# Kernel optimization log

Hardware: AMD Instinct MI355X
Metric: run time of the kernel (lower is better)

The kernel has to match this reference:

```python
import jax, jax.numpy as jnp
import numpy as np

N = 100000
E = 3200000
IN_C = 256
HID = 64
OUT_C = 2
EPS = 1e-5


def setup_inputs() -> dict:
    key = jax.random.key(0)
    ks = jax.random.split(key, 8)
    x = jax.random.normal(ks[0], (N, IN_C), dtype=jnp.float32)
    edge_index = jax.random.randint(ks[1], (2, E), 0, N, dtype=jnp.int64)
    # GCNConv weights (PyG: out = A_hat @ (x W) + b)
    W1 = jax.random.normal(ks[2], (IN_C, HID), dtype=jnp.float32) / np.sqrt(IN_C)
    b1 = jnp.zeros((HID,), dtype=jnp.float32)
    W2 = jax.random.normal(ks[3], (HID, OUT_C), dtype=jnp.float32) / np.sqrt(HID)
    b2 = jnp.zeros((OUT_C,), dtype=jnp.float32)
    # BatchNorm affine params
    g1 = jnp.ones((HID,), dtype=jnp.float32)
    be1 = jnp.zeros((HID,), dtype=jnp.float32)
    g2 = jnp.ones((OUT_C,), dtype=jnp.float32)
    be2 = jnp.zeros((OUT_C,), dtype=jnp.float32)
    # Decoder linear
    Wd = jax.random.normal(ks[4], (OUT_C, IN_C), dtype=jnp.float32) / np.sqrt(OUT_C)
    bd = jnp.zeros((IN_C,), dtype=jnp.float32)
    return {"x": x, "edge_index": edge_index, "W1": W1, "b1": b1, "g1": g1,
            "be1": be1, "W2": W2, "b2": b2, "g2": g2, "be2": be2,
            "Wd": Wd, "bd": bd}


def gcn_conv(x, W, b, src, dst, n):
    # x: [N, Cin] -> [N, Cout]; symmetric-normalized aggregation with self-loops
    xw = x @ W  # [N, Cout]
    loops = jnp.arange(n, dtype=src.dtype)
    s = jnp.concatenate([src, loops])  # [E+N]
    d = jnp.concatenate([dst, loops])
    deg = jax.ops.segment_sum(jnp.ones_like(d, dtype=x.dtype), d, num_segments=n)
    dinv = jax.lax.rsqrt(deg)  # deg >= 1 thanks to self-loops
    norm = dinv[s] * dinv[d]   # [E+N]
    out = jax.ops.segment_sum(norm[:, None] * xw[s], d, num_segments=n)
    return out + b


def batch_norm(x, gamma, beta):
    # training-mode BN over node dim, biased variance (torch semantics)
    mu = jnp.mean(x, axis=0)
    var = jnp.mean(jnp.square(x - mu), axis=0)
    return (x - mu) * jax.lax.rsqrt(var + EPS) * gamma + beta


def reference(x, edge_index, W1, b1, g1, be1, W2, b2, g2, be2, Wd, bd):
    src, dst = edge_index[0], edge_index[1]
    n = x.shape[0]
    h = gcn_conv(x, W1, b1, src, dst, n)
    h = jax.nn.relu(batch_norm(h, g1, be1))
    # dropout: identity (inference)
    z = batch_norm(gcn_conv(h, W2, b2, src, dst, n), g2, be2)
    return z @ Wd + bd  # decoder: [N, IN_C]
```

## Files before the change

### kernel.cpp

```cpp
#include <hip/hip_runtime.h>
#include <hip/hip_bf16.h>

#define NN 100000
#define NE 3200000
#define INC 256
#define HID 64
#define OUTC 2
#define EPSV 1e-5f

#define SCAN_CHUNK 1024
#define NBLK ((NN + SCAN_CHUNK - 1) / SCAN_CHUNK)

#define NBUCK 128
#define BCAP  26000
#define BIN_CHUNK 4096
#define BIN_K 16
#define BIN_GRID ((NE + BIN_CHUNK - 1) / BIN_CHUNK)

#define NHALF 50000

typedef short short8 __attribute__((ext_vector_type(8)));
typedef float f32x4 __attribute__((ext_vector_type(4)));

static __device__ __forceinline__ float bf2f(unsigned short u) {
    return __uint_as_float((unsigned)u << 16);
}
static __device__ __forceinline__ unsigned short f2bf(float f) {
    __hip_bfloat16 hb = __float2bfloat16(f);
    return *(unsigned short*)&hb;
}

__global__ __launch_bounds__(256) void bin_kernel(const int* __restrict__ src,
                                                  const int* __restrict__ dst,
                                                  int* __restrict__ gtail,
                                                  int2* __restrict__ bbuf) {
    __shared__ int bcnt[NBUCK], bbase[NBUCK];
    int t = threadIdx.x;
    if (t < NBUCK) bcnt[t] = 0;
    __syncthreads();
    int base = blockIdx.x * BIN_CHUNK;
    int s[BIN_K], d[BIN_K], sl[BIN_K], bk[BIN_K];
#pragma unroll
    for (int r = 0; r < BIN_K; r++) {
        int i = base + r * 256 + t;
        bool v = i < NE;
        s[r] = v ? src[i] : 0;
        d[r] = v ? dst[i] : 0;
        bk[r] = (int)(((unsigned)d[r] * (unsigned)NBUCK) / (unsigned)NN);
        sl[r] = v ? atomicAdd(&bcnt[bk[r]], 1) : 0;
    }
    __syncthreads();
    if (t < NBUCK) bbase[t] = bcnt[t] ? atomicAdd(&gtail[t], bcnt[t]) : 0;
    __syncthreads();
#pragma unroll
    for (int r = 0; r < BIN_K; r++) {
        int i = base + r * 256 + t;
        if (i < NE) {
            int b = bk[r];
            bbuf[(size_t)b * BCAP + bbase[b] + sl[r]] = make_int2(s[r], d[r]);
        }
    }
}

__global__ __launch_bounds__(256) void hist2_kernel(const int2* __restrict__ bbuf,
                                                    const int* __restrict__ gtail,
                                                    int* __restrict__ cnt) {
    __shared__ int h[800];
    int b = blockIdx.x, t = threadIdx.x;
    int nb = (b * NN + NBUCK - 1) >> 7;
    int ne_ = ((b + 1) * NN + NBUCK - 1) >> 7;
    int range = ne_ - nb;
    for (int i = t; i < range; i += 256) h[i] = 0;
    __syncthreads();
    int ecnt = gtail[b];
    const int2* p = bbuf + (size_t)b * BCAP;
    for (int i = t; i < ecnt; i += 256) {
        int2 e = p[i];
        atomicAdd(&h[e.y - nb], 1);
    }
    __syncthreads();
    for (int i = t; i < range; i += 256) cnt[nb + i] = h[i];
}

__global__ void scan_btot_kernel(const int* __restrict__ cnt, int* __restrict__ btot) {
    __shared__ int red[4];
    int b = blockIdx.x, t = threadIdx.x;
    int base = b * SCAN_CHUNK;
    int v = 0;
    for (int j = t; j < SCAN_CHUNK; j += 256) {
        int idx = base + j;
        v += (idx < NN) ? cnt[idx] : 0;
    }
    for (int o = 32; o; o >>= 1) v += __shfl_xor(v, o);
    int wave = t >> 6, lane = t & 63;
    if (lane == 0) red[wave] = v;
    __syncthreads();
    if (t == 0) btot[b] = red[0] + red[1] + red[2] + red[3];
}

__global__ void scan_boff_kernel(const int* __restrict__ btot, int* __restrict__ boff) {
    __shared__ int wtot[2];
    int t = threadIdx.x;
    int lane = t & 63, wave = t >> 6;
    int v = (t < NBLK) ? btot[t] : 0;
    int s = v;
    for (int o = 1; o < 64; o <<= 1) {
        int u = __shfl_up(s, o);
        if (lane >= o) s += u;
    }
    if (lane == 63) wtot[wave] = s;
    __syncthreads();
    int add = (wave == 1) ? wtot[0] : 0;
    if (t < NBLK) boff[t] = s - v + add;
}

__global__ void scan_rowptr_kernel(const int* __restrict__ cnt, const int* __restrict__ boff,
                                   int* __restrict__ rowptr, float* __restrict__ dinv) {
    __shared__ int wsum[4];
    int b = blockIdx.x, t = threadIdx.x;
    int lane = t & 63, wave = t >> 6;
    int idx = b * SCAN_CHUNK + t * 4;
    int c0 = (idx + 0 < NN) ? cnt[idx + 0] : 0;
    int c1 = (idx + 1 < NN) ? cnt[idx + 1] : 0;
    int c2 = (idx + 2 < NN) ? cnt[idx + 2] : 0;
    int c3 = (idx + 3 < NN) ? cnt[idx + 3] : 0;
    int local = c0 + c1 + c2 + c3;
    int s = local;
    for (int o = 1; o < 64; o <<= 1) {
        int u = __shfl_up(s, o);
        if (lane >= o) s += u;
    }
    if (lane == 63) wsum[wave] = s;
    __syncthreads();
    if (t == 0) {
        int run = 0;
        for (int w = 0; w < 4; w++) { int x = wsum[w]; wsum[w] = run; run += x; }
    }
    __syncthreads();
    int start = boff[b] + wsum[wave] + (s - local);
    if (idx + 0 < NN) { rowptr[idx + 0] = start;                dinv[idx + 0] = rsqrtf((float)(c0 + 1)); }
    if (idx + 1 < NN) { rowptr[idx + 1] = start + c0;           dinv[idx + 1] = rsqrtf((float)(c1 + 1)); }
    if (idx + 2 < NN) { rowptr[idx + 2] = start + c0 + c1;      dinv[idx + 2] = rsqrtf((float)(c2 + 1)); }
    if (idx + 3 < NN) { rowptr[idx + 3] = start + c0 + c1 + c2; dinv[idx + 3] = rsqrtf((float)(c3 + 1)); }
    if (b == 0 && t == 0) rowptr[NN] = NE;
}

__global__ __launch_bounds__(256) void scatter2_kernel(const int2* __restrict__ bbuf,
                                                       const int* __restrict__ gtail,
                                                       const int* __restrict__ rowptr,
                                                       int* __restrict__ e_src) {
    __shared__ int fill[800];
    int b = blockIdx.x, t = threadIdx.x;
    int nb = (b * NN + NBUCK - 1) >> 7;
    int ne_ = ((b + 1) * NN + NBUCK - 1) >> 7;
    int range = ne_ - nb;
    for (int i = t; i < range; i += 256) fill[i] = 0;
    __syncthreads();
    int ecnt = gtail[b];
    const int2* p = bbuf + (size_t)b * BCAP;
    for (int i = t; i < ecnt; i += 256) {
        int2 e = p[i];
        int pos = rowptr[e.y] + atomicAdd(&fill[e.y - nb], 1);
        e_src[pos] = e.x;
    }
}

__global__ __launch_bounds__(256) void wprep_kernel(const float* __restrict__ W1,
                                                    unsigned short* __restrict__ Wtb) {
    int t = blockIdx.x * 256 + threadIdx.x;
    int c = t & 63;
    int k = t >> 6;
    Wtb[c * 256 + k] = f2bf(W1[k * 64 + c]);
}

#define G1_ROWS 32
#define LDP 264
__global__ __launch_bounds__(256) void gemm1_kernel(const float* __restrict__ x,
                                                    const unsigned short* __restrict__ Wtb,
                                                    const float* __restrict__ dinv,
                                                    unsigned short* __restrict__ xw1p) {
    __shared__ unsigned short xt[G1_ROWS * LDP];
    __shared__ unsigned short wt[HID * LDP];
    int t = threadIdx.x;
    size_t base = (size_t)blockIdx.x * G1_ROWS;

    const float4* xg = (const float4*)(x + base * INC);
#pragma unroll
    for (int ii = 0; ii < 8; ii++) {
        int idx4 = ii * 256 + t;
        float4 v = xg[idx4];
        int f = idx4 * 4;
        int row = f >> 8, k = f & 255;
        ushort4 u;
        u.x = f2bf(v.x); u.y = f2bf(v.y); u.z = f2bf(v.z); u.w = f2bf(v.w);
        *(ushort4*)(xt + row * LDP + k) = u;
    }
    const int4* wsrc = (const int4*)Wtb;
#pragma unroll
    for (int ii = 0; ii < 8; ii++) {
        int idx4 = ii * 256 + t;
        int4 v = wsrc[idx4];
        int e16 = idx4 * 8;
        int c = e16 >> 8, k = e16 & 255;
        *(int4*)(wt + c * LDP + k) = v;
    }
    __syncthreads();

    int lane = t & 63;
    int wave = t >> 6;
    int l15 = lane & 15;
    int hi = lane >> 4;
    int rgrp = wave & 1;
    int cgrp = wave >> 1;
    const unsigned short* ap = xt + (rgrp * 16 + l15) * LDP;
    const unsigned short* bp0 = wt + (cgrp * 32 + l15) * LDP;
    const unsigned short* bp1 = bp0 + 16 * LDP;
    f32x4 acc0 = {0.f, 0.f, 0.f, 0.f};
    f32x4 acc1 = {0.f, 0.f, 0.f, 0.f};
#pragma unroll
    for (int kk = 0; kk < 8; kk++) {
        int ko = kk * 32 + hi * 8;
        short8 a  = *(const short8*)(ap + ko);
        short8 b0 = *(const short8*)(bp0 + ko);
        short8 b1 = *(const short8*)(bp1 + ko);
        acc0 = __builtin_amdgcn_mfma_f32_16x16x32_bf16(a, b0, acc0, 0, 0, 0);
        acc1 = __builtin_amdgcn_mfma_f32_16x16x32_bf16(a, b1, acc1, 0, 0, 0);
    }
    unsigned short* p0 = xw1p + (size_t)(cgrp * 2) * NN * 16;
    unsigned short* p1 = p0 + (size_t)NN * 16;
#pragma unroll
    for (int i = 0; i < 4; i++) {
        int grow = (int)base + rgrp * 16 + hi * 4 + i;
        float dv = dinv[grow];
        p0[(size_t)grow * 16 + l15] = f2bf(acc0[i] * dv);
        p1[(size_t)grow * 16 + l15] = f2bf(acc1[i] * dv);
    }
}

__global__ __launch_bounds__(256) void agg1_kernel(const unsigned short* __restrict__ xw1p,
                                                   const int* __restrict__ rowptr,
                                                   const int* __restrict__ e_src,
                                                   const float* __restrict__ dinv,
                                                   const float* __restrict__ b1,
                                                   float* __restrict__ h1p,
                                                   float* __restrict__ sums1) {
    __shared__ float lsum[4][16], lsq[4][16];
    int t = threadIdx.x;
    int lane = t & 63;
    int wave = t >> 6;
    int grp = lane >> 3;
    int cl = lane & 7;
    int cohort = blockIdx.x & 7;
    int q = cohort & 3;
    int h = cohort >> 2;
    const ushort2* plane = (const ushort2*)(xw1p + (size_t)q * NN * 16);
    float* hp = h1p + (size_t)q * NN * 16;
    float bb0 = b1[q * 16 + cl * 2 + 0];
    float bb1 = b1[q * 16 + cl * 2 + 1];
    int gid = ((blockIdx.x >> 3) * 4 + wave) * 8 + grp;
    int dlo = h * NHALF;
    float ssum0 = 0.f, ssq0 = 0.f, ssum1 = 0.f, ssq1 = 0.f;
    for (int d = dlo + gid; d < dlo + NHALF; d += 8192) {
        int beg = rowptr[d], end = rowptr[d + 1];
        float a0 = 0.f, a1 = 0.f;
        int e = beg;
        for (; e + 3 < end; e += 4) {
            int s0 = e_src[e], s1 = e_src[e + 1], s2 = e_src[e + 2], s3 = e_src[e + 3];
            ushort2 u0 = plane[(size_t)s0 * 8 + cl];
            ushort2 u1 = plane[(size_t)s1 * 8 + cl];
            ushort2 u2 = plane[(size_t)s2 * 8 + cl];
            ushort2 u3 = plane[(size_t)s3 * 8 + cl];
            a0 += bf2f(u0.x) + bf2f(u1.x) + bf2f(u2.x) + bf2f(u3.x);
            a1 += bf2f(u0.y) + bf2f(u1.y) + bf2f(u2.y) + bf2f(u3.y);
        }
        for (; e < end; e++) {
            int s = e_src[e];
            ushort2 u = plane[(size_t)s * 8 + cl];
            a0 += bf2f(u.x);
            a1 += bf2f(u.y);
        }
        ushort2 us = plane[(size_t)d * 8 + cl];
        a0 += bf2f(us.x);
        a1 += bf2f(us.y);
        float dv = dinv[d];
        float h0 = a0 * dv + bb0;
        float h1v = a1 * dv + bb1;
        *(float2*)(hp + (size_t)d * 16 + cl * 2) = make_float2(h0, h1v);
        ssum0 += h0; ssq0 += h0 * h0;
        ssum1 += h1v; ssq1 += h1v * h1v;
    }
    ssum0 += __shfl_xor(ssum0, 8);  ssum1 += __shfl_xor(ssum1, 8);
    ssq0  += __shfl_xor(ssq0, 8);   ssq1  += __shfl_xor(ssq1, 8);
    ssum0 += __shfl_xor(ssum0, 16); ssum1 += __shfl_xor(ssum1, 16);
    ssq0  += __shfl_xor(ssq0, 16);  ssq1  += __shfl_xor(ssq1, 16);
    ssum0 += __shfl_xor(ssum0, 32); ssum1 += __shfl_xor(ssum1, 32);
    ssq0  += __shfl_xor(ssq0, 32);  ssq1  += __shfl_xor(ssq1, 32);
    if (grp == 0) {
        lsum[wave][cl * 2] = ssum0; lsum[wave][cl * 2 + 1] = ssum1;
        lsq[wave][cl * 2]  = ssq0;  lsq[wave][cl * 2 + 1]  = ssq1;
    }
    __syncthreads();
    if (t < 16) {
        float S = lsum[0][t] + lsum[1][t] + lsum[2][t] + lsum[3][t];
        float Q = lsq[0][t] + lsq[1][t] + lsq[2][t] + lsq[3][t];
        atomicAdd(&sums1[q * 16 + t], S);
        atomicAdd(&sums1[64 + q * 16 + t], Q);
    }
}

__global__ __launch_bounds__(256) void gemm2_kernel(const float* __restrict__ h1p,
                                                    const float* __restrict__ sums1,
                                                    const float* __restrict__ g1,
                                                    const float* __restrict__ be1,
                                                    const float* __restrict__ W2,
                                                    const float* __restrict__ dinv,
                                                    float* __restrict__ xw2) {
    int lane = threadIdx.x & 63;
    int row = blockIdx.x * 4 + (threadIdx.x >> 6);
    if (row >= NN) return;
    int c = lane;
    const float invn = 1.0f / (float)NN;
    float mu = sums1[c] * invn;
    float var = sums1[64 + c] * invn - mu * mu;
    float sc = g1[c] * rsqrtf(var + EPSV);
    float sh = be1[c] - mu * sc;
    float hv = h1p[(size_t)(c >> 4) * NN * 16 + (size_t)row * 16 + (c & 15)] * sc + sh;
    hv = fmaxf(hv, 0.f);
    float p0 = hv * W2[c * 2 + 0];
    float p1 = hv * W2[c * 2 + 1];
    for (int o = 32; o; o >>= 1) {
        p0 += __shfl_xor(p0, o);
        p1 += __shfl_xor(p1, o);
    }
    if (lane == 0) {
        float dv = dinv[row];
        xw2[(size_t)row * 2 + 0] = p0 * dv;
        xw2[(size_t)row * 2 + 1] = p1 * dv;
    }
}

__global__ __launch_bounds__(256) void agg2_kernel(const float* __restrict__ xw2,
                                                   const int* __restrict__ rowptr,
                                                   const int* __restrict__ e_src,
                                                   const float* __restrict__ dinv,
                                                   const float* __restrict__ b2,
                                                   float* __restrict__ z2,
                                                   float* __restrict__ sums2) {
    __shared__ float red[4][4];
    int t = threadIdx.x;
    int lane = t & 63;
    int wave = t >> 6;
    int gl = lane & 7;
    int d = blockIdx.x * 32 + (t >> 3);
    int beg = rowptr[d], end = rowptr[d + 1];
    float a0 = 0.f, a1 = 0.f;
    int e = beg + gl;
    for (; e + 24 < end; e += 32) {
        int s0 = e_src[e], s1 = e_src[e + 8], s2 = e_src[e + 16], s3 = e_src[e + 24];
        float2 v0 = *(const float2*)(xw2 + (size_t)s0 * 2);
        float2 v1 = *(const float2*)(xw2 + (size_t)s1 * 2);
        float2 v2 = *(const float2*)(xw2 + (size_t)s2 * 2);
        float2 v3 = *(const float2*)(xw2 + (size_t)s3 * 2);
        a0 += v0.x + v1.x + v2.x + v3.x;
        a1 += v0.y + v1.y + v2.y + v3.y;
    }
    for (; e < end; e += 8) {
        int s = e_src[e];
        float2 v = *(const float2*)(xw2 + (size_t)s * 2);
        a0 += v.x;
        a1 += v.y;
    }
    if (gl == 0) {
        float2 sf = *(const float2*)(xw2 + (size_t)d * 2);
        a0 += sf.x;
        a1 += sf.y;
    }
    a0 += __shfl_xor(a0, 1); a1 += __shfl_xor(a1, 1);
    a0 += __shfl_xor(a0, 2); a1 += __shfl_xor(a1, 2);
    a0 += __shfl_xor(a0, 4); a1 += __shfl_xor(a1, 4);
    float dv = dinv[d];
    float z0 = a0 * dv + b2[0];
    float z1 = a1 * dv + b2[1];
    if (gl == 0) *(float2*)(z2 + (size_t)d * 2) = make_float2(z0, z1);
    float s0 = (gl == 0) ? z0 : 0.f;
    float s1 = (gl == 0) ? z1 : 0.f;
    float q0 = (gl == 0) ? z0 * z0 : 0.f;
    float q1 = (gl == 0) ? z1 * z1 : 0.f;
    for (int o = 8; o < 64; o <<= 1) {
        s0 += __shfl_xor(s0, o); s1 += __shfl_xor(s1, o);
        q0 += __shfl_xor(q0, o); q1 += __shfl_xor(q1, o);
    }
    if (lane == 0) { red[wave][0] = s0; red[wave][1] = s1; red[wave][2] = q0; red[wave][3] = q1; }
    __syncthreads();
    if (t < 4) {
        float v = red[0][t] + red[1][t] + red[2][t] + red[3][t];
        atomicAdd(&sums2[(blockIdx.x & 7) * 4 + t], v);
    }
}

__global__ __launch_bounds__(256) void decoder_kernel(const float* __restrict__ z2,
                                                      const float* __restrict__ sums2,
                                                      const float* __restrict__ g2,
                                                      const float* __restrict__ be2,
                                                      const float* __restrict__ Wd,
                                                      const float* __restrict__ bd,
                                                      float* __restrict__ out) {
    int g = blockIdx.x * 256 + threadIdx.x;
    int row = g >> 6;
    int c4 = (g & 63) * 4;
    float t0 = 0.f, t1 = 0.f, t2 = 0.f, t3 = 0.f;
#pragma unroll
    for (int bk = 0; bk < 8; bk++) {
        t0 += sums2[bk * 4 + 0]; t1 += sums2[bk * 4 + 1];
        t2 += sums2[bk * 4 + 2]; t3 += sums2[bk * 4 + 3];
    }
    const float invn = 1.0f / (float)NN;
    float mu0 = t0 * invn, mu1 = t1 * invn;
    float v0 = t2 * invn - mu0 * mu0;
    float v1 = t3 * invn - mu1 * mu1;
    float sc0 = g2[0] * rsqrtf(v0 + EPSV), sh0 = be2[0] - mu0 * sc0;
    float sc1 = g2[1] * rsqrtf(v1 + EPSV), sh1 = be2[1] - mu1 * sc1;
    float zb0 = z2[(size_t)row * 2 + 0] * sc0 + sh0;
    float zb1 = z2[(size_t)row * 2 + 1] * sc1 + sh1;
    float4 w0 = *(const float4*)(Wd + c4);
    float4 w1 = *(const float4*)(Wd + INC + c4);
    float4 bb = *(const float4*)(bd + c4);
    float4 o;
    o.x = zb0 * w0.x + zb1 * w1.x + bb.x;
    o.y = zb0 * w0.y + zb1 * w1.y + bb.y;
    o.z = zb0 * w0.z + zb1 * w1.z + bb.z;
    o.w = zb0 * w0.w + zb1 * w1.w + bb.w;
    *(float4*)(out + (size_t)row * INC + c4) = o;
}

static inline size_t align256(size_t x) { return (x + 255) & ~(size_t)255; }

extern "C" void kernel_launch(void* const* d_in, const int* in_sizes, int n_in,
                              void* d_out, int out_size, void* d_ws, size_t ws_size,
                              hipStream_t stream) {
    const float* x  = (const float*)d_in[0];
    const int*   ei = (const int*)d_in[1];
    const float* W1 = (const float*)d_in[2];
    const float* b1 = (const float*)d_in[3];
    const float* g1 = (const float*)d_in[4];
    const float* be1 = (const float*)d_in[5];
    const float* W2 = (const float*)d_in[6];
    const float* b2 = (const float*)d_in[7];
    const float* g2 = (const float*)d_in[8];
    const float* be2 = (const float*)d_in[9];
    const float* Wd = (const float*)d_in[10];
    const float* bd = (const float*)d_in[11];
    float* out = (float*)d_out;

    const int* src = ei;
    const int* dst = ei + NE;

    char* ws = (char*)d_ws;
    size_t off = 0;
    int* gtail = (int*)(ws + off);      off = align256(off + NBUCK * 4);
    float* sums1 = (float*)(ws + off);  off = align256(off + 128 * 4);
    float* sums2 = (float*)(ws + off);  off = align256(off + 32 * 4);
    size_t zero_bytes = off;
    int* cnt = (int*)(ws + off);        off = align256(off + NN * 4);
    int* rowptr = (int*)(ws + off);     off = align256(off + (NN + 1) * 4);
    float* dinv = (float*)(ws + off);   off = align256(off + NN * 4);
    int* btot = (int*)(ws + off);       off = align256(off + NBLK * 4);
    int* boff = (int*)(ws + off);       off = align256(off + NBLK * 4);
    unsigned short* Wtb = (unsigned short*)(ws + off); off = align256(off + (size_t)HID * INC * 2);
    int2* bbuf = (int2*)(ws + off);     off = align256(off + (size_t)NBUCK * BCAP * 8);
    int* e_src = (int*)(ws + off);      off = align256(off + (size_t)NE * 4 + 64);
    unsigned short* xw1p = (unsigned short*)(ws + off); off = align256(off + (size_t)NN * HID * 2);
    float* h1p = (float*)(ws + off);    off = align256(off + (size_t)NN * HID * 4);
    float* xw2 = (float*)(ws + off);    off = align256(off + (size_t)NN * 2 * 4);
    float* z2 = (float*)(ws + off);     off = align256(off + (size_t)NN * 2 * 4);
    (void)ws_size; (void)in_sizes; (void)n_in; (void)out_size;

    hipMemsetAsync(d_ws, 0, zero_bytes, stream);

    bin_kernel<<<BIN_GRID, 256, 0, stream>>>(src, dst, gtail, bbuf);
    hist2_kernel<<<NBUCK, 256, 0, stream>>>(bbuf, gtail, cnt);
    scan_btot_kernel<<<NBLK, 256, 0, stream>>>(cnt, btot);
    scan_boff_kernel<<<1, 128, 0, stream>>>(btot, boff);
    scan_rowptr_kernel<<<NBLK, 256, 0, stream>>>(cnt, boff, rowptr, dinv);
    scatter2_kernel<<<NBUCK, 256, 0, stream>>>(bbuf, gtail, rowptr, e_src);
    wprep_kernel<<<64, 256, 0, stream>>>(W1, Wtb);
    gemm1_kernel<<<NN / G1_ROWS, 256, 0, stream>>>(x, Wtb, dinv, xw1p);
    agg1_kernel<<<2048, 256, 0, stream>>>(xw1p, rowptr, e_src, dinv, b1, h1p, sums1);
    gemm2_kernel<<<(NN + 3) / 4, 256, 0, stream>>>(h1p, sums1, g1, be1, W2, dinv, xw2);
    agg2_kernel<<<NN * 8 / 256, 256, 0, stream>>>(xw2, rowptr, e_src, dinv, b2, z2, sums2);
    decoder_kernel<<<(NN * HID) / 256, 256, 0, stream>>>(z2, sums2, g2, be2, Wd, bd, out);
}
```

Baseline: 322.0 us.

## Split layer-1 features into two 32-channel planes for wider gathers

The bf16 XW1 intermediate and the fp32 h1 buffer change from four 16-channel planes to two 32-channel planes. Each aggregation thread now gathers 8 bytes (four channels) per neighbour instead of 4 bytes, and each cohort of blocks covers a quarter of the destination nodes instead of a half. The aim is fewer edge-index reads and row-pointer walks per feature and wider, more efficient gather transactions. In exchange each cohort's source plane is twice as large, so it may get less cache reuse, and each thread holds more registers.

Measured after the change: 317.4 us. Within noise of the previous version (-1.4%).

```diff
diff --git a/kernel.cpp b/kernel.cpp
--- a/kernel.cpp
+++ b/kernel.cpp
@@ -17,7 +17,7 @@
 #define BIN_K 16
 #define BIN_GRID ((NE + BIN_CHUNK - 1) / BIN_CHUNK)
 
-#define NHALF 50000
+#define NQUART 25000
 
 typedef short short8 __attribute__((ext_vector_type(8)));
 typedef float f32x4 __attribute__((ext_vector_type(4)));
@@ -178,7 +178,7 @@
 __global__ __launch_bounds__(256) void gemm1_kernel(const float* __restrict__ x,
                                                     const unsigned short* __restrict__ Wtb,
                                                     const float* __restrict__ dinv,
-                                                    unsigned short* __restrict__ xw1p) {
+                                                    unsigned short* __restrict__ xw1h) {
     __shared__ unsigned short xt[G1_ROWS * LDP];
     __shared__ unsigned short wt[HID * LDP];
     int t = threadIdx.x;
@@ -226,89 +226,99 @@
         acc0 = __builtin_amdgcn_mfma_f32_16x16x32_bf16(a, b0, acc0, 0, 0, 0);
         acc1 = __builtin_amdgcn_mfma_f32_16x16x32_bf16(a, b1, acc1, 0, 0, 0);
     }
-    unsigned short* p0 = xw1p + (size_t)(cgrp * 2) * NN * 16;
-    unsigned short* p1 = p0 + (size_t)NN * 16;
+    unsigned short* ph = xw1h + (size_t)cgrp * NN * 32;
 #pragma unroll
     for (int i = 0; i < 4; i++) {
         int grow = (int)base + rgrp * 16 + hi * 4 + i;
         float dv = dinv[grow];
-        p0[(size_t)grow * 16 + l15] = f2bf(acc0[i] * dv);
-        p1[(size_t)grow * 16 + l15] = f2bf(acc1[i] * dv);
-    }
-}
-
-__global__ __launch_bounds__(256) void agg1_kernel(const unsigned short* __restrict__ xw1p,
+        ph[(size_t)grow * 32 + l15]      = f2bf(acc0[i] * dv);
+        ph[(size_t)grow * 32 + l15 + 16] = f2bf(acc1[i] * dv);
+    }
+}
+
+__global__ __launch_bounds__(256) void agg1_kernel(const unsigned short* __restrict__ xw1h,
                                                    const int* __restrict__ rowptr,
                                                    const int* __restrict__ e_src,
                                                    const float* __restrict__ dinv,
                                                    const float* __restrict__ b1,
-                                                   float* __restrict__ h1p,
+                                                   float* __restrict__ h1h,
                                                    float* __restrict__ sums1) {
-    __shared__ float lsum[4][16], lsq[4][16];
+    __shared__ float lsum[4][32], lsq[4][32];
     int t = threadIdx.x;
     int lane = t & 63;
     int wave = t >> 6;
     int grp = lane >> 3;
     int cl = lane & 7;
     int cohort = blockIdx.x & 7;
-    int q = cohort & 3;
-    int h = cohort >> 2;
-    const ushort2* plane = (const ushort2*)(xw1p + (size_t)q * NN * 16);
-    float* hp = h1p + (size_t)q * NN * 16;
-    float bb0 = b1[q * 16 + cl * 2 + 0];
-    float bb1 = b1[q * 16 + cl * 2 + 1];
+    int h = cohort & 1;
+    int dq = cohort >> 1;
+    const ushort4* plane = (const ushort4*)(xw1h + (size_t)h * NN * 32);
+    float* hp = h1h + (size_t)h * NN * 32;
+    float bb0 = b1[h * 32 + cl * 4 + 0];
+    float bb1 = b1[h * 32 + cl * 4 + 1];
+    float bb2 = b1[h * 32 + cl * 4 + 2];
+    float bb3 = b1[h * 32 + cl * 4 + 3];
     int gid = ((blockIdx.x >> 3) * 4 + wave) * 8 + grp;
-    int dlo = h * NHALF;
-    float ssum0 = 0.f, ssq0 = 0.f, ssum1 = 0.f, ssq1 = 0.f;
-    for (int d = dlo + gid; d < dlo + NHALF; d += 8192) {
+    int dlo = dq * NQUART;
+    float ss0 = 0.f, ss1 = 0.f, ss2 = 0.f, ss3 = 0.f;
+    float sq0 = 0.f, sq1 = 0.f, sq2 = 0.f, sq3 = 0.f;
+    for (int d = dlo + gid; d < dlo + NQUART; d += 8192) {
         int beg = rowptr[d], end = rowptr[d + 1];
-        float a0 = 0.f, a1 = 0.f;
+        float a0 = 0.f, a1 = 0.f, a2 = 0.f, a3 = 0.f;
         int e = beg;
         for (; e + 3 < end; e += 4) {
             int s0 = e_src[e], s1 = e_src[e + 1], s2 = e_src[e + 2], s3 = e_src[e + 3];
-            ushort2 u0 = plane[(size_t)s0 * 8 + cl];
-            ushort2 u1 = plane[(size_t)s1 * 8 + cl];
-            ushort2 u2 = plane[(size_t)s2 * 8 + cl];
-            ushort2 u3 = plane[(size_t)s3 * 8 + cl];
+            ushort4 u0 = plane[(size_t)s0 * 8 + cl];
+            ushort4 u1 = plane[(size_t)s1 * 8 + cl];
+            ushort4 u2 = plane[(size_t)s2 * 8 + cl];
+            ushort4 u3 = plane[(size_t)s3 * 8 + cl];
             a0 += bf2f(u0.x) + bf2f(u1.x) + bf2f(u2.x) + bf2f(u3.x);
             a1 += bf2f(u0.y) + bf2f(u1.y) + bf2f(u2.y) + bf2f(u3.y);
+            a2 += bf2f(u0.z) + bf2f(u1.z) + bf2f(u2.z) + bf2f(u3.z);
+            a3 += bf2f(u0.w) + bf2f(u1.w) + bf2f(u2.w) + bf2f(u3.w);
         }
         for (; e < end; e++) {
             int s = e_src[e];
-            ushort2 u = plane[(size_t)s * 8 + cl];
-            a0 += bf2f(u.x);
-            a1 += bf2f(u.y);
+            ushort4 u = plane[(size_t)s * 8 + cl];
+            a0 += bf2f(u.x); a1 += bf2f(u.y); a2 += bf2f(u.z); a3 += bf2f(u.w);
         }
-        ushort2 us = plane[(size_t)d * 8 + cl];
-        a0 += bf2f(us.x);
-        a1 += bf2f(us.y);
+        ushort4 us = plane[(size_t)d * 8 + cl];
+        a0 += bf2f(us.x); a1 += bf2f(us.y); a2 += bf2f(us.z); a3 += bf2f(us.w);
         float dv = dinv[d];
         float h0 = a0 * dv + bb0;
         float h1v = a1 * dv + bb1;
-        *(float2*)(hp + (size_t)d * 16 + cl * 2) = make_float2(h0, h1v);
-        ssum0 += h0; ssq0 += h0 * h0;
-        ssum1 += h1v; ssq1 += h1v * h1v;
-    }
-    ssum0 += __shfl_xor(ssum0, 8);  ssum1 += __shfl_xor(ssum1, 8);
-    ssq0  += __shfl_xor(ssq0, 8);   ssq1  += __shfl_xor(ssq1, 8);
-    ssum0 += __shfl_xor(ssum0, 16); ssum1 += __shfl_xor(ssum1, 16);
-    ssq0  += __shfl_xor(ssq0, 16);  ssq1  += __shfl_xor(ssq1, 16);
-    ssum0 += __shfl_xor(ssum0, 32); ssum1 += __shfl_xor(ssum1, 32);
-    ssq0  += __shfl_xor(ssq0, 32);  ssq1  += __shfl_xor(ssq1, 32);
+        float h2 = a2 * dv + bb2;
+        float h3 = a3 * dv + bb3;
+        f32x4 hv = {h0, h1v, h2, h3};
+        *(f32x4*)(hp + (size_t)d * 32 + cl * 4) = hv;
+        ss0 += h0; sq0 += h0 * h0;
+        ss1 += h1v; sq1 += h1v * h1v;
+        ss2 += h2; sq2 += h2 * h2;
+        ss3 += h3; sq3 += h3 * h3;
+    }
+#pragma unroll
+    for (int o = 8; o < 64; o <<= 1) {
+        ss0 += __shfl_xor(ss0, o); sq0 += __shfl_xor(sq0, o);
+        ss1 += __shfl_xor(ss1, o); sq1 += __shfl_xor(sq1, o);
+        ss2 += __shfl_xor(ss2, o); sq2 += __shfl_xor(sq2, o);
+        ss3 += __shfl_xor(ss3, o); sq3 += __shfl_xor(sq3, o);
+    }
     if (grp == 0) {
-        lsum[wave][cl * 2] = ssum0; lsum[wave][cl * 2 + 1] = ssum1;
-        lsq[wave][cl * 2]  = ssq0;  lsq[wave][cl * 2 + 1]  = ssq1;
-    }
-    __syncthreads();
-    if (t < 16) {
+        lsum[wave][cl * 4 + 0] = ss0; lsq[wave][cl * 4 + 0] = sq0;
+        lsum[wave][cl * 4 + 1] = ss1; lsq[wave][cl * 4 + 1] = sq1;
+        lsum[wave][cl * 4 + 2] = ss2; lsq[wave][cl * 4 + 2] = sq2;
+        lsum[wave][cl * 4 + 3] = ss3; lsq[wave][cl * 4 + 3] = sq3;
+    }
+    __syncthreads();
+    if (t < 32) {
         float S = lsum[0][t] + lsum[1][t] + lsum[2][t] + lsum[3][t];
         float Q = lsq[0][t] + lsq[1][t] + lsq[2][t] + lsq[3][t];
-        atomicAdd(&sums1[q * 16 + t], S);
-        atomicAdd(&sums1[64 + q * 16 + t], Q);
-    }
-}
-
-__global__ __launch_bounds__(256) void gemm2_kernel(const float* __restrict__ h1p,
+        atomicAdd(&sums1[h * 32 + t], S);
+        atomicAdd(&sums1[64 + h * 32 + t], Q);
+    }
+}
+
+__global__ __launch_bounds__(256) void gemm2_kernel(const float* __restrict__ h1h,
                                                     const float* __restrict__ sums1,
                                                     const float* __restrict__ g1,
                                                     const float* __restrict__ be1,
@@ -324,7 +334,7 @@
     float var = sums1[64 + c] * invn - mu * mu;
     float sc = g1[c] * rsqrtf(var + EPSV);
     float sh = be1[c] - mu * sc;
-    float hv = h1p[(size_t)(c >> 4) * NN * 16 + (size_t)row * 16 + (c & 15)] * sc + sh;
+    float hv = h1h[(size_t)(c >> 5) * NN * 32 + (size_t)row * 32 + (c & 31)] * sc + sh;
     hv = fmaxf(hv, 0.f);
     float p0 = hv * W2[c * 2 + 0];
     float p1 = hv * W2[c * 2 + 1];
@@ -469,8 +479,8 @@
     unsigned short* Wtb = (unsigned short*)(ws + off); off = align256(off + (size_t)HID * INC * 2);
     int2* bbuf = (int2*)(ws + off);     off = align256(off + (size_t)NBUCK * BCAP * 8);
     int* e_src = (int*)(ws + off);      off = align256(off + (size_t)NE * 4 + 64);
-    unsigned short* xw1p = (unsigned short*)(ws + off); off = align256(off + (size_t)NN * HID * 2);
-    float* h1p = (float*)(ws + off);    off = align256(off + (size_t)NN * HID * 4);
+    unsigned short* xw1h = (unsigned short*)(ws + off); off = align256(off + (size_t)NN * HID * 2);
+    float* h1h = (float*)(ws + off);    off = align256(off + (size_t)NN * HID * 4);
     float* xw2 = (float*)(ws + off);    off = align256(off + (size_t)NN * 2 * 4);
     float* z2 = (float*)(ws + off);     off = align256(off + (size_t)NN * 2 * 4);
     (void)ws_size; (void)in_sizes; (void)n_in; (void)out_size;
@@ -484,9 +494,9 @@
     scan_rowptr_kernel<<<NBLK, 256, 0, stream>>>(cnt, boff, rowptr, dinv);
     scatter2_kernel<<<NBUCK, 256, 0, stream>>>(bbuf, gtail, rowptr, e_src);
     wprep_kernel<<<64, 256, 0, stream>>>(W1, Wtb);
-    gemm1_kernel<<<NN / G1_ROWS, 256, 0, stream>>>(x, Wtb, dinv, xw1p);
-    agg1_kernel<<<2048, 256, 0, stream>>>(xw1p, rowptr, e_src, dinv, b1, h1p, sums1);
-    gemm2_kernel<<<(NN + 3) / 4, 256, 0, stream>>>(h1p, sums1, g1, be1, W2, dinv, xw2);
+    gemm1_kernel<<<NN / G1_ROWS, 256, 0, stream>>>(x, Wtb, dinv, xw1h);
+    agg1_kernel<<<2048, 256, 0, stream>>>(xw1h, rowptr, e_src, dinv, b1, h1h, sums1);
+    gemm2_kernel<<<(NN + 3) / 4, 256, 0, stream>>>(h1h, sums1, g1, be1, W2, dinv, xw2);
     agg2_kernel<<<NN * 8 / 256, 256, 0, stream>>>(xw2, rowptr, e_src, dinv, b2, z2, sums2);
     decoder_kernel<<<(NN * HID) / 256, 256, 0, stream>>>(z2, sums2, g2, be2, Wd, bd, out);
 }
```
